# Kernel tuning notes

Measured on AMD Instinct MI355X. Metric: run time of the kernel, lower is better.

## Reference

```python
import jax, jax.numpy as jnp
import numpy as np

DEPTH = 2
NW = 4          # number of wires (qubits), fixed by 2x2 patches
NP = 14 * 14    # patches per image
NUM_CLASSES = 10


def _ry(theta):
    c = jnp.cos(theta / 2).astype(jnp.complex64)
    s = jnp.sin(theta / 2).astype(jnp.complex64)
    return jnp.stack([jnp.stack([c, -s], -1), jnp.stack([s, c], -1)], -2)


def _rx(theta):
    c = jnp.cos(theta / 2).astype(jnp.complex64)
    s = (-1j) * jnp.sin(theta / 2).astype(jnp.complex64)
    return jnp.stack([jnp.stack([c, s], -1), jnp.stack([s, c], -1)], -2)


def _rz(theta):
    em = jnp.exp(-0.5j * theta.astype(jnp.complex64))
    ep = jnp.exp(0.5j * theta.astype(jnp.complex64))
    z = jnp.zeros_like(em)
    return jnp.stack([jnp.stack([em, z], -1), jnp.stack([z, ep], -1)], -2)


def _apply1(state, mat, wire):
    # state: (N,2,2,2,2); mat: (2,2) shared or (N,2,2) per-patch
    s = jnp.moveaxis(state, 1 + wire, -1)
    if mat.ndim == 2:
        s = jnp.einsum('...i,ji->...j', s, mat)
    else:
        s = jnp.einsum('n...i,nji->n...j', s, mat)
    return jnp.moveaxis(s, -1, 1 + wire)


def _cnot(state, c, t):
    a0 = jnp.take(state, 0, axis=1 + c)
    a1 = jnp.take(state, 1, axis=1 + c)
    t_ax = 1 + t - (1 if t > c else 0)   # target axis index after control removed
    a1 = jnp.flip(a1, axis=t_ax)
    return jnp.stack([a0, a1], axis=1 + c)


def _circuit(angles, params):
    # angles: (N,4) RY-encoded patch pixels; params: (DEPTH,NW,3)
    N = angles.shape[0]
    state = jnp.zeros((N, 16), jnp.complex64).at[:, 0].set(1.0).reshape(N, 2, 2, 2, 2)
    for w in range(NW):
        state = _apply1(state, _ry(angles[:, w]), w)
    for d in range(DEPTH):
        for w in range(NW):
            state = _apply1(state, _rx(params[d, w, 0]), w)
            state = _apply1(state, _ry(params[d, w, 1]), w)
            state = _apply1(state, _rz(params[d, w, 2]), w)
        for w in range(NW - 1):
            state = _cnot(state, w, w + 1)
        state = _cnot(state, NW - 1, 0)
    probs = state.real ** 2 + state.imag ** 2   # (N,2,2,2,2)
    feats = []
    for w in range(NW):
        p = jnp.moveaxis(probs, 1 + w, 1).reshape(N, 2, 8)
        feats.append(p[:, 0].sum(-1) - p[:, 1].sum(-1))  # <Z_w>
    return jnp.stack(feats, -1)                  # (N,4)


def setup_inputs() -> dict:
    key = jax.random.key(0)
    k1, k2, k3 = jax.random.split(key, 3)
    B = 4096
    x = jax.random.uniform(k1, (B, 1, 28, 28), jnp.float32)
    params = jax.random.normal(k2, (DEPTH, NW, 3), jnp.float32)
    W = jax.random.normal(k3, (NUM_CLASSES, NW * NP), jnp.float32) * 0.02
    b = jnp.zeros((NUM_CLASSES,), jnp.float32)
    return {"x": x, "params": params, "W": W, "b": b}


def reference(x, params, W, b):
    B = x.shape[0]
    # extract all 196 2x2 patches, row-major within each patch (matches view(bsz,-1))
    patches = x[:, 0].reshape(B, 14, 2, 14, 2).transpose(0, 1, 3, 2, 4).reshape(B * NP, 4)
    feats = _circuit(patches, params).reshape(B, NP * NW)  # (B,784)
    logits = feats @ W.T + b
    return jax.nn.log_softmax(logits, axis=-1)
```

## Files before the change

kernel.cpp:

```cpp
#include <hip/hip_runtime.h>
#include <hip/hip_bf16.h>

#define NPATCH 196

typedef float f2 __attribute__((ext_vector_type(2)));

__global__ __launch_bounds__(256) void quanv_setup(const float* __restrict__ P,
                                                   float* __restrict__ C) {
  __shared__ float gc[24], gs[24];
  __shared__ float Ur[8][2][2], Ui[8][2][2];
  __shared__ float Sr[2][16][16], Si[2][16][16];
  __shared__ float A[4][16][16];
  __shared__ float B0[4][3][8][8];
  __shared__ float B1[4][3][3][4][4];
  __shared__ float B2[4][3][3][3][2][2];
  const int tid = threadIdx.x;
  const int row = tid >> 4, col = tid & 15;

  if (tid < 24) {
    float s, c;
    __sincosf(0.5f * P[tid], &s, &c);
    gc[tid] = c; gs[tid] = s;
  }
  Sr[0][row][col] = (row == col) ? 1.0f : 0.0f;
  Si[0][row][col] = 0.0f;
  __syncthreads();

  if (tid < 8) {
    const int base = tid * 3;
    const float c1 = gc[base], s1 = gs[base];
    const float c2 = gc[base + 1], s2 = gs[base + 1];
    const float c3 = gc[base + 2], s3 = gs[base + 2];
    const float m00r = c2 * c1, m00i = s2 * s1;
    const float m01r = -s2 * c1, m01i = -c2 * s1;
    const float m10r = s2 * c1, m10i = -c2 * s1;
    const float m11r = c2 * c1, m11i = -s2 * s1;
    Ur[tid][0][0] = c3 * m00r + s3 * m00i;  Ui[tid][0][0] = c3 * m00i - s3 * m00r;
    Ur[tid][0][1] = c3 * m01r + s3 * m01i;  Ui[tid][0][1] = c3 * m01i - s3 * m01r;
    Ur[tid][1][0] = c3 * m10r - s3 * m10i;  Ui[tid][1][0] = c3 * m10i + s3 * m10r;
    Ur[tid][1][1] = c3 * m11r - s3 * m11i;  Ui[tid][1][1] = c3 * m11i + s3 * m11r;
  }
  __syncthreads();

  int cur = 0;
  for (int d = 0; d < 2; ++d) {
    for (int w = 0; w < 4; ++w) {
      const int gi = d * 4 + w;
      const int m = 8 >> w;
      const int bit = (row & m) ? 1 : 0;
      const int par = row ^ m;
      const int r0 = bit ? par : row, r1 = bit ? row : par;
      const float a_r = Sr[cur][r0][col], a_i = Si[cur][r0][col];
      const float b_r = Sr[cur][r1][col], b_i = Si[cur][r1][col];
      const float u0r = Ur[gi][bit][0], u0i = Ui[gi][bit][0];
      const float u1r = Ur[gi][bit][1], u1i = Ui[gi][bit][1];
      const float rn = u0r * a_r - u0i * a_i + u1r * b_r - u1i * b_i;
      const float in_ = u0r * a_i + u0i * a_r + u1r * b_i + u1i * b_r;
      Sr[cur ^ 1][row][col] = rn;
      Si[cur ^ 1][row][col] = in_;
      cur ^= 1;
      __syncthreads();
    }
    if (d == 0) {
      int k = row;
      k ^= (k & 1) ? 8 : 0;
      k ^= (k & 2) ? 1 : 0;
      k ^= (k & 4) ? 2 : 0;
      k ^= (k & 8) ? 4 : 0;
      const float pr_ = Sr[cur][k][col], pi_ = Si[cur][k][col];
      Sr[cur ^ 1][row][col] = pr_;
      Si[cur ^ 1][row][col] = pi_;
      cur ^= 1;
      __syncthreads();
    }
  }

  {
    const int i = row, j = col;
    float s0 = 0, s1 = 0, s2 = 0, s3 = 0;
#pragma unroll
    for (int k = 0; k < 16; ++k) {
      int gk = k;
      gk ^= (gk & 1) ? 8 : 0;
      gk ^= (gk & 2) ? 1 : 0;
      gk ^= (gk & 4) ? 2 : 0;
      gk ^= (gk & 8) ? 4 : 0;
      const float pr = Sr[cur][gk][i] * Sr[cur][gk][j] + Si[cur][gk][i] * Si[cur][gk][j];
      s0 += (k & 8) ? -pr : pr;
      s1 += (k & 4) ? -pr : pr;
      s2 += (k & 2) ? -pr : pr;
      s3 += (k & 1) ? -pr : pr;
    }
    A[0][i][j] = s0; A[1][i][j] = s1; A[2][i][j] = s2; A[3][i][j] = s3;
  }
  __syncthreads();

  {
    const int w = tid >> 6, ip = (tid >> 3) & 7, jp = tid & 7;
    const float a00 = A[w][ip][jp],     a11 = A[w][ip + 8][jp + 8];
    const float a01 = A[w][ip][jp + 8], a10 = A[w][ip + 8][jp];
    B0[w][0][ip][jp] = 0.5f * (a00 + a11);
    B0[w][1][ip][jp] = 0.5f * (a00 - a11);
    B0[w][2][ip][jp] = 0.5f * (a01 + a10);
  }
  __syncthreads();
  if (tid < 192) {
    const int w = tid / 48, a0 = (tid / 16) % 3, ii = (tid >> 2) & 3, jj = tid & 3;
    const float a00 = B0[w][a0][ii][jj],     a11 = B0[w][a0][ii + 4][jj + 4];
    const float a01 = B0[w][a0][ii][jj + 4], a10 = B0[w][a0][ii + 4][jj];
    B1[w][a0][0][ii][jj] = 0.5f * (a00 + a11);
    B1[w][a0][1][ii][jj] = 0.5f * (a00 - a11);
    B1[w][a0][2][ii][jj] = 0.5f * (a01 + a10);
  }
  __syncthreads();
  if (tid < 144) {
    const int w = tid / 36, a0 = (tid / 12) % 3, a1 = (tid / 4) % 3;
    const int i3 = (tid >> 1) & 1, j3 = tid & 1;
    const float a00 = B1[w][a0][a1][i3][j3],     a11 = B1[w][a0][a1][i3 + 2][j3 + 2];
    const float a01 = B1[w][a0][a1][i3][j3 + 2], a10 = B1[w][a0][a1][i3 + 2][j3];
    B2[w][a0][a1][0][i3][j3] = 0.5f * (a00 + a11);
    B2[w][a0][a1][1][i3][j3] = 0.5f * (a00 - a11);
    B2[w][a0][a1][2][i3][j3] = 0.5f * (a01 + a10);
  }
  __syncthreads();
  if (tid < 108) {
    const int w = tid / 27, r = tid % 27;
    const int a0 = r / 9, a1 = (r / 3) % 3, a2 = r % 3;
    const float a00 = B2[w][a0][a1][a2][0][0], a11 = B2[w][a0][a1][a2][1][1];
    const float a01 = B2[w][a0][a1][a2][0][1], a10 = B2[w][a0][a1][a2][1][0];
    const int base = (3 * a0 + a1) * 9 + 3 * a2;
    C[(base + 0) * 4 + w] = 0.5f * (a00 + a11);
    C[(base + 1) * 4 + w] = 0.5f * (a00 - a11);
    C[(base + 2) * 4 + w] = 0.5f * (a01 + a10);
  }
}

__global__ __launch_bounds__(256) void quanv_main(const float* __restrict__ x,
                                                  const float* __restrict__ W,
                                                  const float* __restrict__ bias,
                                                  const float* __restrict__ C,
                                                  float* __restrict__ out) {
  __shared__ float red2[49][10];
  __shared__ float logits[10];
  __shared__ float snorm;
  const int tid = threadIdx.x;
  const int b = blockIdx.x;

  float lg[10];
#pragma unroll
  for (int k = 0; k < 10; ++k) lg[k] = 0.0f;

  if (tid < NPATCH) {
    const int pi = tid / 14, pj = tid - pi * 14;
    const float* px = x + b * 784 + pi * 56 + pj * 2;
    const float2 r0 = *reinterpret_cast<const float2*>(px);
    const float2 r1 = *reinterpret_cast<const float2*>(px + 28);
    float c0, s0, c1, s1, c2, s2, c3, s3;
    __sincosf(r0.x, &s0, &c0);
    __sincosf(r0.y, &s1, &c1);
    __sincosf(r1.x, &s2, &c2);
    __sincosf(r1.y, &s3, &c3);
    const float m01s[9] = {1.0f, c1, s1, c0, c0 * c1, c0 * s1, s0, s0 * c1, s0 * s1};
    const float m23s[9] = {1.0f, c3, s3, c2, c2 * c3, c2 * s3, s2, s2 * c3, s2 * s3};
    f2 m23b[9];
#pragma unroll
    for (int q = 0; q < 9; ++q) m23b[q] = (f2){m23s[q], m23s[q]};

    f2 f01 = {0.0f, 0.0f}, f23 = {0.0f, 0.0f};
    const f2* C2 = reinterpret_cast<const f2*>(C);
#pragma unroll
    for (int a = 0; a < 9; ++a) {
      f2 t01 = {0.0f, 0.0f}, t23 = {0.0f, 0.0f};
#pragma unroll
      for (int q = 0; q < 9; ++q) {
        const int idx = (a * 9 + q) * 2;
        t01 += C2[idx] * m23b[q];
        t23 += C2[idx + 1] * m23b[q];
      }
      f01 += t01 * m01s[a];
      f23 += t23 * m01s[a];
    }
    const float f0 = f01.x, f1 = f01.y, f2v = f23.x, f3 = f23.y;

    const float* Wp = W + tid * 4;
#pragma unroll
    for (int k = 0; k < 10; ++k) {
      const float4 wv = *reinterpret_cast<const float4*>(Wp + k * 784);
      lg[k] = f0 * wv.x + f1 * wv.y + f2v * wv.z + f3 * wv.w;
    }
  }

#pragma unroll
  for (int k = 0; k < 10; ++k) {
    lg[k] += __shfl_xor(lg[k], 1);
    lg[k] += __shfl_xor(lg[k], 2);
  }
  if (tid < NPATCH) {
    const int g = tid >> 2, sub = tid & 3;
#pragma unroll
    for (int k = 0; k < 10; ++k)
      if ((k & 3) == sub) red2[g][k] = lg[k];
  }
  __syncthreads();
  if (tid < 10) {
    float s = bias[tid];
    for (int g2 = 0; g2 < 49; ++g2) s += red2[g2][tid];
    logits[tid] = s;
  }
  __syncthreads();
  if (tid == 0) {
    float m = logits[0];
#pragma unroll
    for (int k = 1; k < 10; ++k) m = fmaxf(m, logits[k]);
    float se = 0;
#pragma unroll
    for (int k = 0; k < 10; ++k) se += expf(logits[k] - m);
    snorm = m + logf(se);
  }
  __syncthreads();
  if (tid < 10) out[b * 10 + tid] = logits[tid] - snorm;
}

extern "C" void kernel_launch(void* const* d_in, const int* in_sizes, int n_in,
                              void* d_out, int out_size, void* d_ws, size_t ws_size,
                              hipStream_t stream) {
  const float* x = (const float*)d_in[0];
  const float* P = (const float*)d_in[1];
  const float* W = (const float*)d_in[2];
  const float* bias = (const float*)d_in[3];
  float* out = (float*)d_out;
  float* C = (float*)d_ws;
  const int B = out_size / 10;

  quanv_setup<<<1, 256, 0, stream>>>(P, C);
  quanv_main<<<B, 256, 0, stream>>>(x, W, bias, C, out);
}
```

Baseline: 24.43 us.

## Fuse coefficient setup into main kernel and process two images per block

Removes the separate single-block setup kernel. Every block now recomputes the circuit coefficient table into shared memory and then evaluates two images. This eliminates one launch and the serial dependency between kernels, and it moves the coefficient reads from global memory to shared memory. In exchange every block repeats the setup work, including its many barrier-separated phases, and uses more shared memory, which may lower occupancy.

```diff
diff --git a/kernel.cpp b/kernel.cpp
--- a/kernel.cpp
+++ b/kernel.cpp
@@ -5,8 +5,12 @@
 
 typedef float f2 __attribute__((ext_vector_type(2)));
 
-__global__ __launch_bounds__(256) void quanv_setup(const float* __restrict__ P,
-                                                   float* __restrict__ C) {
+__global__ __launch_bounds__(256) void quanv_fused(const float* __restrict__ x,
+                                                   const float* __restrict__ P,
+                                                   const float* __restrict__ W,
+                                                   const float* __restrict__ bias,
+                                                   float* __restrict__ out,
+                                                   int B) {
   __shared__ float gc[24], gs[24];
   __shared__ float Ur[8][2][2], Ui[8][2][2];
   __shared__ float Sr[2][16][16], Si[2][16][16];
@@ -14,6 +18,10 @@
   __shared__ float B0[4][3][8][8];
   __shared__ float B1[4][3][3][4][4];
   __shared__ float B2[4][3][3][3][2][2];
+  __shared__ float4 Cl[81];
+  __shared__ float red2[2][49][10];
+  __shared__ float logits[2][10];
+  __shared__ float snorm[2];
   const int tid = threadIdx.x;
   const int row = tid >> 4, col = tid & 15;
 
@@ -129,96 +137,105 @@
     const float a00 = B2[w][a0][a1][a2][0][0], a11 = B2[w][a0][a1][a2][1][1];
     const float a01 = B2[w][a0][a1][a2][0][1], a10 = B2[w][a0][a1][a2][1][0];
     const int base = (3 * a0 + a1) * 9 + 3 * a2;
-    C[(base + 0) * 4 + w] = 0.5f * (a00 + a11);
-    C[(base + 1) * 4 + w] = 0.5f * (a00 - a11);
-    C[(base + 2) * 4 + w] = 0.5f * (a01 + a10);
-  }
-}
-
-__global__ __launch_bounds__(256) void quanv_main(const float* __restrict__ x,
-                                                  const float* __restrict__ W,
-                                                  const float* __restrict__ bias,
-                                                  const float* __restrict__ C,
-                                                  float* __restrict__ out) {
-  __shared__ float red2[49][10];
-  __shared__ float logits[10];
-  __shared__ float snorm;
-  const int tid = threadIdx.x;
-  const int b = blockIdx.x;
-
-  float lg[10];
-#pragma unroll
-  for (int k = 0; k < 10; ++k) lg[k] = 0.0f;
-
+    float* Cf = reinterpret_cast<float*>(Cl);
+    Cf[(base + 0) * 4 + w] = 0.5f * (a00 + a11);
+    Cf[(base + 1) * 4 + w] = 0.5f * (a00 - a11);
+    Cf[(base + 2) * 4 + w] = 0.5f * (a01 + a10);
+  }
+  __syncthreads();
+
+  float f[2][4];
+#pragma unroll
+  for (int img = 0; img < 2; ++img)
+#pragma unroll
+    for (int w = 0; w < 4; ++w) f[img][w] = 0.0f;
+
+  const int pi = tid / 14, pj = tid - pi * 14;
+#pragma unroll
+  for (int img = 0; img < 2; ++img) {
+    const int b = blockIdx.x * 2 + img;
+    if (tid < NPATCH && b < B) {
+      const float* px = x + b * 784 + pi * 56 + pj * 2;
+      const float2 r0 = *reinterpret_cast<const float2*>(px);
+      const float2 r1 = *reinterpret_cast<const float2*>(px + 28);
+      float c0, s0, c1, s1, c2, s2, c3, s3;
+      __sincosf(r0.x, &s0, &c0);
+      __sincosf(r0.y, &s1, &c1);
+      __sincosf(r1.x, &s2, &c2);
+      __sincosf(r1.y, &s3, &c3);
+      const float m01s[9] = {1.0f, c1, s1, c0, c0 * c1, c0 * s1, s0, s0 * c1, s0 * s1};
+      const float m23s[9] = {1.0f, c3, s3, c2, c2 * c3, c2 * s3, s2, s2 * c3, s2 * s3};
+      f2 m23b[9];
+#pragma unroll
+      for (int q = 0; q < 9; ++q) m23b[q] = (f2){m23s[q], m23s[q]};
+
+      f2 f01 = {0.0f, 0.0f}, f23 = {0.0f, 0.0f};
+#pragma unroll
+      for (int a = 0; a < 9; ++a) {
+        f2 t01 = {0.0f, 0.0f}, t23 = {0.0f, 0.0f};
+#pragma unroll
+        for (int q = 0; q < 9; ++q) {
+          const float4 cc = Cl[a * 9 + q];
+          t01 += (f2){cc.x, cc.y} * m23b[q];
+          t23 += (f2){cc.z, cc.w} * m23b[q];
+        }
+        f01 += t01 * m01s[a];
+        f23 += t23 * m01s[a];
+      }
+      f[img][0] = f01.x; f[img][1] = f01.y; f[img][2] = f23.x; f[img][3] = f23.y;
+    }
+  }
+
+  float lg[2][10];
+#pragma unroll
+  for (int k = 0; k < 10; ++k) { lg[0][k] = 0.0f; lg[1][k] = 0.0f; }
   if (tid < NPATCH) {
-    const int pi = tid / 14, pj = tid - pi * 14;
-    const float* px = x + b * 784 + pi * 56 + pj * 2;
-    const float2 r0 = *reinterpret_cast<const float2*>(px);
-    const float2 r1 = *reinterpret_cast<const float2*>(px + 28);
-    float c0, s0, c1, s1, c2, s2, c3, s3;
-    __sincosf(r0.x, &s0, &c0);
-    __sincosf(r0.y, &s1, &c1);
-    __sincosf(r1.x, &s2, &c2);
-    __sincosf(r1.y, &s3, &c3);
-    const float m01s[9] = {1.0f, c1, s1, c0, c0 * c1, c0 * s1, s0, s0 * c1, s0 * s1};
-    const float m23s[9] = {1.0f, c3, s3, c2, c2 * c3, c2 * s3, s2, s2 * c3, s2 * s3};
-    f2 m23b[9];
-#pragma unroll
-    for (int q = 0; q < 9; ++q) m23b[q] = (f2){m23s[q], m23s[q]};
-
-    f2 f01 = {0.0f, 0.0f}, f23 = {0.0f, 0.0f};
-    const f2* C2 = reinterpret_cast<const f2*>(C);
-#pragma unroll
-    for (int a = 0; a < 9; ++a) {
-      f2 t01 = {0.0f, 0.0f}, t23 = {0.0f, 0.0f};
-#pragma unroll
-      for (int q = 0; q < 9; ++q) {
-        const int idx = (a * 9 + q) * 2;
-        t01 += C2[idx] * m23b[q];
-        t23 += C2[idx + 1] * m23b[q];
-      }
-      f01 += t01 * m01s[a];
-      f23 += t23 * m01s[a];
-    }
-    const float f0 = f01.x, f1 = f01.y, f2v = f23.x, f3 = f23.y;
-
     const float* Wp = W + tid * 4;
 #pragma unroll
     for (int k = 0; k < 10; ++k) {
       const float4 wv = *reinterpret_cast<const float4*>(Wp + k * 784);
-      lg[k] = f0 * wv.x + f1 * wv.y + f2v * wv.z + f3 * wv.w;
+      lg[0][k] = f[0][0] * wv.x + f[0][1] * wv.y + f[0][2] * wv.z + f[0][3] * wv.w;
+      lg[1][k] = f[1][0] * wv.x + f[1][1] * wv.y + f[1][2] * wv.z + f[1][3] * wv.w;
     }
   }
 
 #pragma unroll
   for (int k = 0; k < 10; ++k) {
-    lg[k] += __shfl_xor(lg[k], 1);
-    lg[k] += __shfl_xor(lg[k], 2);
+    lg[0][k] += __shfl_xor(lg[0][k], 1);
+    lg[0][k] += __shfl_xor(lg[0][k], 2);
+    lg[1][k] += __shfl_xor(lg[1][k], 1);
+    lg[1][k] += __shfl_xor(lg[1][k], 2);
   }
   if (tid < NPATCH) {
     const int g = tid >> 2, sub = tid & 3;
 #pragma unroll
     for (int k = 0; k < 10; ++k)
-      if ((k & 3) == sub) red2[g][k] = lg[k];
-  }
-  __syncthreads();
-  if (tid < 10) {
-    float s = bias[tid];
-    for (int g2 = 0; g2 < 49; ++g2) s += red2[g2][tid];
-    logits[tid] = s;
-  }
-  __syncthreads();
-  if (tid == 0) {
-    float m = logits[0];
-#pragma unroll
-    for (int k = 1; k < 10; ++k) m = fmaxf(m, logits[k]);
+      if ((k & 3) == sub) { red2[0][g][k] = lg[0][k]; red2[1][g][k] = lg[1][k]; }
+  }
+  __syncthreads();
+
+  if (tid < 20) {
+    const int img = tid / 10, k = tid - img * 10;
+    float s = bias[k];
+    for (int g = 0; g < 49; ++g) s += red2[img][g][k];
+    logits[img][k] = s;
+  }
+  __syncthreads();
+  if (tid < 2) {
+    float m = logits[tid][0];
+#pragma unroll
+    for (int k = 1; k < 10; ++k) m = fmaxf(m, logits[tid][k]);
     float se = 0;
 #pragma unroll
-    for (int k = 0; k < 10; ++k) se += expf(logits[k] - m);
-    snorm = m + logf(se);
-  }
-  __syncthreads();
-  if (tid < 10) out[b * 10 + tid] = logits[tid] - snorm;
+    for (int k = 0; k < 10; ++k) se += expf(logits[tid][k] - m);
+    snorm[tid] = m + logf(se);
+  }
+  __syncthreads();
+  if (tid < 20) {
+    const int img = tid / 10, k = tid - img * 10;
+    const int b = blockIdx.x * 2 + img;
+    if (b < B) out[b * 10 + k] = logits[img][k] - snorm[img];
+  }
 }
 
 extern "C" void kernel_launch(void* const* d_in, const int* in_sizes, int n_in,
@@ -229,9 +246,7 @@
   const float* W = (const float*)d_in[2];
   const float* bias = (const float*)d_in[3];
   float* out = (float*)d_out;
-  float* C = (float*)d_ws;
   const int B = out_size / 10;
 
-  quanv_setup<<<1, 256, 0, stream>>>(P, C);
-  quanv_main<<<B, 256, 0, stream>>>(x, W, bias, C, out);
+  quanv_fused<<<(B + 1) / 2, 256, 0, stream>>>(x, P, W, bias, out, B);
 }
```

After: 30.56 us. +25.1%, slower.

## Map one wavefront per image with full-wave shuffle reduction and LDS-staged coefficients

Applied to the files above, without the earlier changes.

Each 64-lane wavefront now processes one image, looping over its 196 patches four at a time, and each block handles four images. This replaces the block-wide shared-memory reduction and its several __syncthreads with a pure butterfly shuffle reduction, and computes the log-softmax redundantly in registers. The 81 float4 coefficient entries are staged in LDS instead of being read from global memory per thread. It removes idle threads (60 of 256 were unused) and barrier overhead, but gives each thread more serial work and cuts the block count by four.

```diff
diff --git a/kernel.cpp b/kernel.cpp
--- a/kernel.cpp
+++ b/kernel.cpp
@@ -139,86 +139,92 @@
                                                   const float* __restrict__ W,
                                                   const float* __restrict__ bias,
                                                   const float* __restrict__ C,
-                                                  float* __restrict__ out) {
-  __shared__ float red2[49][10];
-  __shared__ float logits[10];
-  __shared__ float snorm;
+                                                  float* __restrict__ out,
+                                                  int B) {
+  __shared__ float4 Cl[81];
   const int tid = threadIdx.x;
-  const int b = blockIdx.x;
+  if (tid < 81) Cl[tid] = reinterpret_cast<const float4*>(C)[tid];
+  __syncthreads();
+
+  const int wid = tid >> 6, lane = tid & 63;
+  const int b = blockIdx.x * 4 + wid;
+  if (b >= B) return;
+  const float* xb = x + b * 784;
 
   float lg[10];
 #pragma unroll
   for (int k = 0; k < 10; ++k) lg[k] = 0.0f;
 
-  if (tid < NPATCH) {
-    const int pi = tid / 14, pj = tid - pi * 14;
-    const float* px = x + b * 784 + pi * 56 + pj * 2;
-    const float2 r0 = *reinterpret_cast<const float2*>(px);
-    const float2 r1 = *reinterpret_cast<const float2*>(px + 28);
-    float c0, s0, c1, s1, c2, s2, c3, s3;
-    __sincosf(r0.x, &s0, &c0);
-    __sincosf(r0.y, &s1, &c1);
-    __sincosf(r1.x, &s2, &c2);
-    __sincosf(r1.y, &s3, &c3);
-    const float m01s[9] = {1.0f, c1, s1, c0, c0 * c1, c0 * s1, s0, s0 * c1, s0 * s1};
-    const float m23s[9] = {1.0f, c3, s3, c2, c2 * c3, c2 * s3, s2, s2 * c3, s2 * s3};
-    f2 m23b[9];
-#pragma unroll
-    for (int q = 0; q < 9; ++q) m23b[q] = (f2){m23s[q], m23s[q]};
-
-    f2 f01 = {0.0f, 0.0f}, f23 = {0.0f, 0.0f};
-    const f2* C2 = reinterpret_cast<const f2*>(C);
-#pragma unroll
-    for (int a = 0; a < 9; ++a) {
-      f2 t01 = {0.0f, 0.0f}, t23 = {0.0f, 0.0f};
-#pragma unroll
-      for (int q = 0; q < 9; ++q) {
-        const int idx = (a * 9 + q) * 2;
-        t01 += C2[idx] * m23b[q];
-        t23 += C2[idx + 1] * m23b[q];
+#pragma unroll
+  for (int t = 0; t < 4; ++t) {
+    const int p = lane + 64 * t;
+    if (t < 3 || p < NPATCH) {
+      const int pi = p / 14, pj = p - pi * 14;
+      const float* px = xb + pi * 56 + pj * 2;
+      const float2 r0 = *reinterpret_cast<const float2*>(px);
+      const float2 r1 = *reinterpret_cast<const float2*>(px + 28);
+      float c0, s0, c1, s1, c2, s2, c3, s3;
+      __sincosf(r0.x, &s0, &c0);
+      __sincosf(r0.y, &s1, &c1);
+      __sincosf(r1.x, &s2, &c2);
+      __sincosf(r1.y, &s3, &c3);
+      const float m01s[9] = {1.0f, c1, s1, c0, c0 * c1, c0 * s1, s0, s0 * c1, s0 * s1};
+      const float m23s[9] = {1.0f, c3, s3, c2, c2 * c3, c2 * s3, s2, s2 * c3, s2 * s3};
+      f2 m23b[9];
+#pragma unroll
+      for (int q = 0; q < 9; ++q) m23b[q] = (f2){m23s[q], m23s[q]};
+
+      f2 f01 = {0.0f, 0.0f}, f23 = {0.0f, 0.0f};
+#pragma unroll
+      for (int a = 0; a < 9; ++a) {
+        f2 t01 = {0.0f, 0.0f}, t23 = {0.0f, 0.0f};
+#pragma unroll
+        for (int q = 0; q < 9; ++q) {
+          const float4 cc = Cl[a * 9 + q];
+          t01 += (f2){cc.x, cc.y} * m23b[q];
+          t23 += (f2){cc.z, cc.w} * m23b[q];
+        }
+        f01 += t01 * m01s[a];
+        f23 += t23 * m01s[a];
       }
-      f01 += t01 * m01s[a];
-      f23 += t23 * m01s[a];
-    }
-    const float f0 = f01.x, f1 = f01.y, f2v = f23.x, f3 = f23.y;
-
-    const float* Wp = W + tid * 4;
-#pragma unroll
-    for (int k = 0; k < 10; ++k) {
-      const float4 wv = *reinterpret_cast<const float4*>(Wp + k * 784);
-      lg[k] = f0 * wv.x + f1 * wv.y + f2v * wv.z + f3 * wv.w;
+
+      const float* Wp = W + p * 4;
+#pragma unroll
+      for (int k = 0; k < 10; ++k) {
+        const float4 wv = *reinterpret_cast<const float4*>(Wp + k * 784);
+        lg[k] += f01.x * wv.x + f01.y * wv.y + f23.x * wv.z + f23.y * wv.w;
+      }
     }
   }
 
 #pragma unroll
   for (int k = 0; k < 10; ++k) {
-    lg[k] += __shfl_xor(lg[k], 1);
-    lg[k] += __shfl_xor(lg[k], 2);
-  }
-  if (tid < NPATCH) {
-    const int g = tid >> 2, sub = tid & 3;
-#pragma unroll
-    for (int k = 0; k < 10; ++k)
-      if ((k & 3) == sub) red2[g][k] = lg[k];
-  }
-  __syncthreads();
-  if (tid < 10) {
-    float s = bias[tid];
-    for (int g2 = 0; g2 < 49; ++g2) s += red2[g2][tid];
-    logits[tid] = s;
-  }
-  __syncthreads();
-  if (tid == 0) {
-    float m = logits[0];
-#pragma unroll
-    for (int k = 1; k < 10; ++k) m = fmaxf(m, logits[k]);
-    float se = 0;
-#pragma unroll
-    for (int k = 0; k < 10; ++k) se += expf(logits[k] - m);
-    snorm = m + logf(se);
-  }
-  __syncthreads();
-  if (tid < 10) out[b * 10 + tid] = logits[tid] - snorm;
+    float v = lg[k];
+    v += __shfl_xor(v, 1);
+    v += __shfl_xor(v, 2);
+    v += __shfl_xor(v, 4);
+    v += __shfl_xor(v, 8);
+    v += __shfl_xor(v, 16);
+    v += __shfl_xor(v, 32);
+    lg[k] = v;
+  }
+#pragma unroll
+  for (int k = 0; k < 10; ++k) lg[k] += bias[k];
+
+  float m = lg[0];
+#pragma unroll
+  for (int k = 1; k < 10; ++k) m = fmaxf(m, lg[k]);
+  float se = 0.0f;
+#pragma unroll
+  for (int k = 0; k < 10; ++k) se += expf(lg[k] - m);
+  const float sn = m + logf(se);
+
+  if (lane < 10) {
+    float v = lg[0];
+#pragma unroll
+    for (int k = 1; k < 10; ++k) v = (lane == k) ? lg[k] : v;
+    out[b * 10 + lane] = v - sn;
+  }
 }
 
 extern "C" void kernel_launch(void* const* d_in, const int* in_sizes, int n_in,
@@ -233,5 +239,5 @@
   const int B = out_size / 10;
 
   quanv_setup<<<1, 256, 0, stream>>>(P, C);
-  quanv_main<<<B, 256, 0, stream>>>(x, W, bias, C, out);
+  quanv_main<<<(B + 3) / 4, 256, 0, stream>>>(x, W, bias, C, out, B);
 }
```

Result: slower. 44.68 us (+82.9%).

## Process two images per block to reuse C and W loads, parallelize logit reduction

Applied to the files above, without the earlier changes.

Each block now handles two images, so every load of the 81 precomputed C coefficients and of the W rows feeds two sets of accumulations. This halves the grid size and the per-image cost of those loads. The inner contraction changes from a factored two-stage sum to a flat 81-term float4 sum with the m01*m23 products formed per term, which adds multiplies. The serial 49-term logit reduction is split into a two-stage parallel reduction, and softmax is computed per thread. Register pressure doubles, and launch bounds now request 4 blocks.

```diff
diff --git a/kernel.cpp b/kernel.cpp
--- a/kernel.cpp
+++ b/kernel.cpp
@@ -2,8 +2,6 @@
 #include <hip/hip_bf16.h>
 
 #define NPATCH 196
-
-typedef float f2 __attribute__((ext_vector_type(2)));
 
 __global__ __launch_bounds__(256) void quanv_setup(const float* __restrict__ P,
                                                    float* __restrict__ C) {
@@ -135,90 +133,119 @@
   }
 }
 
-__global__ __launch_bounds__(256) void quanv_main(const float* __restrict__ x,
-                                                  const float* __restrict__ W,
-                                                  const float* __restrict__ bias,
-                                                  const float* __restrict__ C,
-                                                  float* __restrict__ out) {
-  __shared__ float red2[49][10];
-  __shared__ float logits[10];
-  __shared__ float snorm;
+__global__ __launch_bounds__(256, 4) void quanv_main(const float* __restrict__ x,
+                                                     const float* __restrict__ W,
+                                                     const float* __restrict__ bias,
+                                                     const float* __restrict__ C,
+                                                     float* __restrict__ out,
+                                                     int B) {
+  __shared__ float red2[2][49][10];
+  __shared__ float red3[2][10][7];
+  __shared__ float logits[2][10];
   const int tid = threadIdx.x;
-  const int b = blockIdx.x;
-
-  float lg[10];
-#pragma unroll
-  for (int k = 0; k < 10; ++k) lg[k] = 0.0f;
+  const int b0 = blockIdx.x * 2;
+  const int b1 = (b0 + 1 < B) ? (b0 + 1) : b0;
+
+  float lgA[10], lgB[10];
+#pragma unroll
+  for (int k = 0; k < 10; ++k) { lgA[k] = 0.0f; lgB[k] = 0.0f; }
 
   if (tid < NPATCH) {
     const int pi = tid / 14, pj = tid - pi * 14;
-    const float* px = x + b * 784 + pi * 56 + pj * 2;
-    const float2 r0 = *reinterpret_cast<const float2*>(px);
-    const float2 r1 = *reinterpret_cast<const float2*>(px + 28);
-    float c0, s0, c1, s1, c2, s2, c3, s3;
-    __sincosf(r0.x, &s0, &c0);
-    __sincosf(r0.y, &s1, &c1);
-    __sincosf(r1.x, &s2, &c2);
-    __sincosf(r1.y, &s3, &c3);
-    const float m01s[9] = {1.0f, c1, s1, c0, c0 * c1, c0 * s1, s0, s0 * c1, s0 * s1};
-    const float m23s[9] = {1.0f, c3, s3, c2, c2 * c3, c2 * s3, s2, s2 * c3, s2 * s3};
-    f2 m23b[9];
-#pragma unroll
-    for (int q = 0; q < 9; ++q) m23b[q] = (f2){m23s[q], m23s[q]};
-
-    f2 f01 = {0.0f, 0.0f}, f23 = {0.0f, 0.0f};
-    const f2* C2 = reinterpret_cast<const f2*>(C);
+    const int off = pi * 56 + pj * 2;
+    const float* pxA = x + b0 * 784 + off;
+    const float* pxB = x + b1 * 784 + off;
+    const float2 a0 = *reinterpret_cast<const float2*>(pxA);
+    const float2 a1 = *reinterpret_cast<const float2*>(pxA + 28);
+    const float2 b0v = *reinterpret_cast<const float2*>(pxB);
+    const float2 b1v = *reinterpret_cast<const float2*>(pxB + 28);
+
+    float ca0, sa0, ca1, sa1, ca2, sa2, ca3, sa3;
+    __sincosf(a0.x, &sa0, &ca0);
+    __sincosf(a0.y, &sa1, &ca1);
+    __sincosf(a1.x, &sa2, &ca2);
+    __sincosf(a1.y, &sa3, &ca3);
+    float cb0, sb0, cb1, sb1, cb2, sb2, cb3, sb3;
+    __sincosf(b0v.x, &sb0, &cb0);
+    __sincosf(b0v.y, &sb1, &cb1);
+    __sincosf(b1v.x, &sb2, &cb2);
+    __sincosf(b1v.y, &sb3, &cb3);
+
+    const float m01A[9] = {1.0f, ca1, sa1, ca0, ca0 * ca1, ca0 * sa1, sa0, sa0 * ca1, sa0 * sa1};
+    const float m23A[9] = {1.0f, ca3, sa3, ca2, ca2 * ca3, ca2 * sa3, sa2, sa2 * ca3, sa2 * sa3};
+    const float m01B[9] = {1.0f, cb1, sb1, cb0, cb0 * cb1, cb0 * sb1, sb0, sb0 * cb1, sb0 * sb1};
+    const float m23B[9] = {1.0f, cb3, sb3, cb2, cb2 * cb3, cb2 * sb3, sb2, sb2 * cb3, sb2 * sb3};
+
+    float f0A = 0, f1A = 0, f2A = 0, f3A = 0;
+    float f0B = 0, f1B = 0, f2B = 0, f3B = 0;
+    const float4* C4 = reinterpret_cast<const float4*>(C);
 #pragma unroll
     for (int a = 0; a < 9; ++a) {
-      f2 t01 = {0.0f, 0.0f}, t23 = {0.0f, 0.0f};
 #pragma unroll
       for (int q = 0; q < 9; ++q) {
-        const int idx = (a * 9 + q) * 2;
-        t01 += C2[idx] * m23b[q];
-        t23 += C2[idx + 1] * m23b[q];
+        const float4 cc = C4[a * 9 + q];
+        const float prA = m01A[a] * m23A[q];
+        const float prB = m01B[a] * m23B[q];
+        f0A += cc.x * prA; f1A += cc.y * prA; f2A += cc.z * prA; f3A += cc.w * prA;
+        f0B += cc.x * prB; f1B += cc.y * prB; f2B += cc.z * prB; f3B += cc.w * prB;
       }
-      f01 += t01 * m01s[a];
-      f23 += t23 * m01s[a];
-    }
-    const float f0 = f01.x, f1 = f01.y, f2v = f23.x, f3 = f23.y;
+    }
 
     const float* Wp = W + tid * 4;
 #pragma unroll
     for (int k = 0; k < 10; ++k) {
       const float4 wv = *reinterpret_cast<const float4*>(Wp + k * 784);
-      lg[k] = f0 * wv.x + f1 * wv.y + f2v * wv.z + f3 * wv.w;
+      lgA[k] = f0A * wv.x + f1A * wv.y + f2A * wv.z + f3A * wv.w;
+      lgB[k] = f0B * wv.x + f1B * wv.y + f2B * wv.z + f3B * wv.w;
     }
   }
 
 #pragma unroll
   for (int k = 0; k < 10; ++k) {
-    lg[k] += __shfl_xor(lg[k], 1);
-    lg[k] += __shfl_xor(lg[k], 2);
+    lgA[k] += __shfl_xor(lgA[k], 1);
+    lgA[k] += __shfl_xor(lgA[k], 2);
+    lgB[k] += __shfl_xor(lgB[k], 1);
+    lgB[k] += __shfl_xor(lgB[k], 2);
   }
   if (tid < NPATCH) {
     const int g = tid >> 2, sub = tid & 3;
 #pragma unroll
     for (int k = 0; k < 10; ++k)
-      if ((k & 3) == sub) red2[g][k] = lg[k];
-  }
-  __syncthreads();
-  if (tid < 10) {
-    float s = bias[tid];
-    for (int g2 = 0; g2 < 49; ++g2) s += red2[g2][tid];
-    logits[tid] = s;
-  }
-  __syncthreads();
-  if (tid == 0) {
-    float m = logits[0];
-#pragma unroll
-    for (int k = 1; k < 10; ++k) m = fmaxf(m, logits[k]);
-    float se = 0;
-#pragma unroll
-    for (int k = 0; k < 10; ++k) se += expf(logits[k] - m);
-    snorm = m + logf(se);
-  }
-  __syncthreads();
-  if (tid < 10) out[b * 10 + tid] = logits[tid] - snorm;
+      if ((k & 3) == sub) { red2[0][g][k] = lgA[k]; red2[1][g][k] = lgB[k]; }
+  }
+  __syncthreads();
+
+  if (tid < 140) {
+    const int img = tid / 70, r = tid - img * 70;
+    const int k = r / 7, part = r - k * 7;
+    float s = 0.0f;
+#pragma unroll
+    for (int j = 0; j < 7; ++j) s += red2[img][part * 7 + j][k];
+    red3[img][k][part] = s;
+  }
+  __syncthreads();
+
+  if (tid < 20) {
+    const int img = tid / 10, k = tid - img * 10;
+    float s = bias[k];
+#pragma unroll
+    for (int j = 0; j < 7; ++j) s += red3[img][k][j];
+    logits[img][k] = s;
+  }
+  __syncthreads();
+
+  if (tid < 20) {
+    const int img = tid / 10, k = tid - img * 10;
+    float m = logits[img][0];
+#pragma unroll
+    for (int kk = 1; kk < 10; ++kk) m = fmaxf(m, logits[img][kk]);
+    float se = 0.0f;
+#pragma unroll
+    for (int kk = 0; kk < 10; ++kk) se += expf(logits[img][kk] - m);
+    const float sn = m + logf(se);
+    const int b = b0 + img;
+    if (b < B) out[b * 10 + k] = logits[img][k] - sn;
+  }
 }
 
 extern "C" void kernel_launch(void* const* d_in, const int* in_sizes, int n_in,
@@ -233,5 +260,5 @@
   const int B = out_size / 10;
 
   quanv_setup<<<1, 256, 0, stream>>>(P, C);
-  quanv_main<<<B, 256, 0, stream>>>(x, W, bias, C, out);
+  quanv_main<<<(B + 1) / 2, 256, 0, stream>>>(x, W, bias, C, out, B);
 }
```

Measured after the change: 28.19 us. 15.4% more time.
